# Optimization experiments

Measured on AMD Instinct MI355X. Metric: run time of the kernel, lower is better.

## Reference

```python
import jax, jax.numpy as jnp
import numpy as np

K = 1023   # kernel_size == embedding_dim
H = 16     # out_channels (filters per sample)
E = 256    # num_embeddings
T = 8      # num_tokens
CC = 0.25  # commitment cost
EPS = np.float32(np.finfo(np.float32).eps)
DN = ('NCH', 'OIH', 'NCH')


def setup_inputs() -> dict:
    key = jax.random.key(0)
    ks = jax.random.split(key, 10)
    B, C, L = 8, 1, 8184
    D_ff = 2 * E
    X = jax.random.normal(ks[0], (B, C, L), jnp.float32)
    embedding = jax.random.uniform(ks[1], (E, K), jnp.float32, -1.0 / E, 1.0 / E)
    ffn_w1 = jax.random.normal(ks[2], (E, D_ff), jnp.float32) * 0.02
    ffn_b1 = jnp.zeros((D_ff,), jnp.float32)
    ffn_w2 = jax.random.normal(ks[3], (D_ff, E), jnp.float32) * 0.02
    ffn_b2 = jnp.zeros((E,), jnp.float32)
    ln_g = jnp.ones((E,), jnp.float32)
    ln_b = jnp.zeros((E,), jnp.float32)
    cls_w = jax.random.normal(ks[4], (E, 10), jnp.float32) * 0.02
    cls_b = jnp.zeros((10,), jnp.float32)
    return dict(X=X, embedding=embedding, ffn_w1=ffn_w1, ffn_b1=ffn_b1,
                ffn_w2=ffn_w2, ffn_b2=ffn_b2, ln_g=ln_g, ln_b=ln_b,
                cls_w=cls_w, cls_b=cls_b)


def _autocov(f):
    # f: [..., K]. FFT-based autocovariance of hann-windowed, max-normalized frame.
    n = f.shape[-1]
    fmax = jnp.max(jnp.abs(f), axis=-1, keepdims=True)
    fmax = jnp.where(fmax == 0, EPS, fmax)
    win = 0.5 * (1.0 - jnp.cos(2.0 * jnp.pi * jnp.arange(n, dtype=jnp.float32) / n))
    xw = f * win / fmax
    spec = jnp.abs(jnp.fft.rfft(xw, n=n) ** 2)   # |rfft(x)^2| == |rfft(x)|^2
    return jnp.fft.ifftshift(jnp.fft.irfft(spec, n=n), axes=-1)


def reference(X, embedding, ffn_w1, ffn_b1, ffn_w2, ffn_b2, ln_g, ln_b, cls_w, cls_b):
    B, C, L = X.shape
    # ---- encoder: extract frames at fixed linspace positions, autocovariance ----
    Lp = ((L + K - 1) // K) * K          # PadForConv(zero) length (no-op here)
    end = Lp - K - 1 - K
    positions = jnp.linspace(0.0, float(end), H).astype(jnp.int32)
    idx = positions[:, None] + jnp.arange(K)          # (H, K)
    frames = X[:, :, idx]                             # (B, C, H, K) gather
    Z = _autocov(jnp.transpose(frames, (0, 2, 1, 3)))  # (B, H, C, K)
    # ---- VQ: pairwise distances + argmin + codebook lookup ----
    flat = Z.reshape(-1, K)                           # (B*H*C, K)
    d = (jnp.sum(flat ** 2, axis=1, keepdims=True)
         + jnp.sum(embedding ** 2, axis=1)
         - 2.0 * flat @ embedding.T)                  # (B*H*C, E)
    codes = jnp.argmin(d, axis=1)
    enc = jax.nn.one_hot(codes, E, dtype=flat.dtype)
    quant = (enc @ embedding).reshape(Z.shape)
    sg = jax.lax.stop_gradient
    e_loss = jnp.mean((sg(quant) - Z) ** 2)
    q_loss = jnp.mean((quant - sg(Z)) ** 2)
    vq_loss = q_loss + CC * e_loss
    quant_st = Z + sg(quant - Z)                      # straight-through
    avg = jnp.mean(enc, axis=0)
    perplexity = jnp.exp(-jnp.sum(avg * jnp.log(avg + EPS)))
    # ---- decoder: every sample's filter bank convolved with the whole batch ----
    fmerged = quant_st.reshape(B * H, C, K)           # merge per-sample banks
    out = jax.lax.conv_general_dilated(X, fmerged, (1,), 'SAME',
                                       dimension_numbers=DN)  # (B, B*H, L)
    out = out.reshape(B, B, H, L)                     # (batch b, filter-sample i, k, L)
    sq = (out - X[:, None, :, :]) ** 2                # C==1 broadcast
    # sum_i mean_k mse_{b,l} == mean over (b,k,l) then sum over i
    recon_loss = jnp.sum(jnp.mean(sq, axis=(0, 2, 3)))
    # ---- project: conv with codebook as filters ----
    pfilt = jnp.broadcast_to(embedding[:, None, :], (E, C, K))
    proj = jax.lax.conv_general_dilated(X, pfilt, (1,), 'VALID',
                                        dimension_numbers=DN)  # (B, E, Lo)
    Lo = proj.shape[-1]
    pad = ((Lo + T - 1) // T) * T - Lo                # PadForConv(mean)
    m = jnp.mean(proj, axis=-1, keepdims=True)
    proj = jnp.concatenate([proj, jnp.broadcast_to(m, (B, E, pad))], axis=-1)
    # ---- classify ----
    x = proj.reshape(B, E, T, -1).transpose(0, 2, 3, 1)  # (B, T, t, E)
    x = jnp.max(x, axis=2)                               # (B, T, E)
    mu = jnp.mean(x, axis=-1, keepdims=True)
    var = jnp.var(x, axis=-1, keepdims=True)
    xn = (x - mu) / jnp.sqrt(var + 1e-5) * ln_g + ln_b
    hdd = jax.nn.relu(xn @ ffn_w1 + ffn_b1) @ ffn_w2 + ffn_b2
    feat = jnp.mean(hdd, axis=1)                         # (B, E)
    logits = feat @ cls_w + cls_b
    return (logits, vq_loss, recon_loss, perplexity)
```

## Files before the change

kernel.cpp:

```cpp
#include <hip/hip_runtime.h>

#define KK 1023
#define LL 8184
#define LO 7162
#define XPS 10240
#define EPSF 1.1920928955078125e-07f
#define NEG_INF (-3.4028234663852886e+38f)

typedef short bf16x8 __attribute__((ext_vector_type(8)));
typedef float f32x4 __attribute__((ext_vector_type(4)));

__device__ __constant__ int c_pos[16] = {0,409,818,1227,1636,2045,2454,2863,
                                         3273,3682,4091,4500,4909,5318,5727,6137};

__device__ __forceinline__ unsigned short f2bf(float f) {
    unsigned u = __float_as_uint(f);
    unsigned r = (u + 0x7FFFu + ((u >> 16) & 1u)) >> 16;
    return (unsigned short)r;
}
__device__ __forceinline__ int fenc(float f) {
    int u = __float_as_int(f);
    return u >= 0 ? u : (~u) ^ 0x80000000;
}
__device__ __forceinline__ float fdec(int k) {
    int u = k >= 0 ? k : ~(k ^ 0x80000000);
    return __int_as_float(u);
}
__device__ __forceinline__ void gl2lds16(const void* g, void* l) {
    __builtin_amdgcn_global_load_lds(
        (const __attribute__((address_space(1))) void*)g,
        (__attribute__((address_space(3))) void*)l, 16, 0, 0);
}

__global__ __launch_bounds__(256) void k_pa(const float* __restrict__ X,
                                            const float* __restrict__ emb,
                                            unsigned short* __restrict__ Xpad,
                                            unsigned short* __restrict__ Xodd,
                                            unsigned short* __restrict__ Ebf,
                                            float* __restrict__ Etf,
                                            float* __restrict__ enorm,
                                            int* __restrict__ hist,
                                            int* __restrict__ cmax,
                                            float* __restrict__ Z) {
    __shared__ __align__(16) float xw[2048];
    __shared__ float red[256];
    const int q = blockIdx.x;
    const int tid = threadIdx.x;
    if (q < 256) {
        const int fi = q >> 1, half = q & 1;
        const int b = fi >> 4, h = fi & 15;
        const float* xp = X + b * LL + c_pos[h];
        float lmax = 0.f;
        for (int j = tid; j < KK; j += 256) {
            float v = xp[j];
            xw[j] = v;
            lmax = fmaxf(lmax, fabsf(v));
        }
        red[tid] = lmax;
        __syncthreads();
        for (int off = 128; off; off >>= 1) {
            if (tid < off) red[tid] = fmaxf(red[tid], red[tid + off]);
            __syncthreads();
        }
        float fmx = red[0];
        if (fmx == 0.f) fmx = EPSF;
        __syncthreads();
        for (int j = tid; j < KK; j += 256) {
            float v = xw[j];
            float win = 0.5f * (1.0f - cosf(6.28318530717958647692f * (float)j / 1023.0f));
            float w = v * win / fmx;
            xw[j] = w;
            xw[j + KK] = w;
        }
        __syncthreads();

        if (tid < 128) {
            const int m = half * 512 + 4 * tid;
            const int mh = m >> 1;
            const int mq4 = mh >> 1;
            const float2* X2 = (const float2*)xw;
            const float4* X4 = (const float4*)xw;
            float a0 = 0.f, a1 = 0.f, a2 = 0.f, a3 = 0.f;
            float2 W0 = X2[mh], W1 = X2[mh + 1], W2 = X2[mh + 2], W3 = X2[mh + 3];
            for (int jh = 0; jh < 510; jh += 2) {
                float4 nw = X4[mq4 + (jh >> 1) + 2];
                float4 xj = X4[jh >> 1];
                a0 = fmaf(xj.x, W0.x, a0);
                a0 = fmaf(xj.y, W0.y, a0);
                a0 = fmaf(xj.z, W1.x, a0);
                a0 = fmaf(xj.w, W1.y, a0);
                a1 = fmaf(xj.x, W0.y, a1);
                a1 = fmaf(xj.y, W1.x, a1);
                a1 = fmaf(xj.z, W1.y, a1);
                a1 = fmaf(xj.w, W2.x, a1);
                a2 = fmaf(xj.x, W1.x, a2);
                a2 = fmaf(xj.y, W1.y, a2);
                a2 = fmaf(xj.z, W2.x, a2);
                a2 = fmaf(xj.w, W2.y, a2);
                a3 = fmaf(xj.x, W1.y, a3);
                a3 = fmaf(xj.y, W2.x, a3);
                a3 = fmaf(xj.z, W2.y, a3);
                a3 = fmaf(xj.w, W3.x, a3);
                W0 = W2; W1 = W3;
                W2 = make_float2(nw.x, nw.y);
                W3 = make_float2(nw.z, nw.w);
            }
            {
                float2 xj = X2[510];
                a0 = fmaf(xj.x, W0.x, a0);
                a0 = fmaf(xj.y, W0.y, a0);
                a1 = fmaf(xj.x, W0.y, a1);
                a1 = fmaf(xj.y, W1.x, a1);
                a2 = fmaf(xj.x, W1.x, a2);
                a2 = fmaf(xj.y, W1.y, a2);
                a3 = fmaf(xj.x, W1.y, a3);
                a3 = fmaf(xj.y, W2.x, a3);
            }
            float xt = xw[1022];
            a0 = fmaf(xt, W1.x, a0);
            a1 = fmaf(xt, W1.y, a1);
            a2 = fmaf(xt, W2.x, a2);
            a3 = fmaf(xt, W2.y, a3);

            float* zrow = Z + fi * KK;
            float av[4] = {a0, a1, a2, a3};
#pragma unroll
            for (int qq = 0; qq < 4; ++qq) {
                int mmq = m + qq;
                if (mmq < KK) {
                    int i0 = mmq + 512; if (i0 >= KK) i0 -= KK;
                    zrow[i0] = av[qq];
                }
            }
        }
    } else if (q < 288) {
        const int qq = q - 256;
        const int b = qq >> 2, seg = qq & 3;
        for (int i = seg * 2560 + tid; i < (seg + 1) * 2560; i += 256) {
            unsigned short v = 0, vo = 0;
            if (i >= 512 && i < 512 + LL) v = f2bf(X[b * LL + (i - 512)]);
            const int i1 = i + 1;
            if (i1 >= 512 && i1 < 512 + LL) vo = f2bf(X[b * LL + (i1 - 512)]);
            Xpad[b * XPS + i] = v;
            Xodd[b * XPS + i] = vo;
        }
    } else if (q < 544) {
        const int e = q - 288;
        const float* er = emb + e * KK;
        float nrm = 0.f;
        for (int k = tid; k < 1024; k += 256) {
            float v = (k < KK) ? er[k] : 0.f;
            Ebf[e * 1024 + k] = (k < KK) ? f2bf(v) : (unsigned short)0;
            Etf[(k >> 2) * 1024 + e * 4 + (k & 3)] = v;
            nrm = fmaf(v, v, nrm);
        }
        red[tid] = nrm;
        __syncthreads();
        for (int off = 128; off; off >>= 1) {
            if (tid < off) red[tid] += red[tid + off];
            __syncthreads();
        }
        if (tid == 0) enorm[e] = red[0];
    } else {
        const int i = (q - 544) * 256 + tid;
        cmax[i] = INT_MIN;
        if (q == 544) hist[tid] = 0;
    }
}

__global__ __launch_bounds__(256, 4) void kA(const float* __restrict__ Z,
                                             const float4* __restrict__ Et4,
                                             const float* __restrict__ enorm,
                                             const float* __restrict__ emb,
                                             int* __restrict__ codes,
                                             int* __restrict__ hist,
                                             float* __restrict__ vq_part,
                                             const unsigned short* __restrict__ Xpad,
                                             const unsigned short* __restrict__ Xodd,
                                             const unsigned short* __restrict__ Ebf,
                                             float* __restrict__ psum_part,
                                             int* __restrict__ cmax) {
    __shared__ __align__(16) char smem[32768];
    const int tid = threadIdx.x;
    const int bi = blockIdx.x;
    if (bi < 128) {
        float* zl  = (float*)smem;
        float* zm2 = (float*)(smem + 4096);
        float* rv  = (float*)(smem + 8192);
        int*   ri  = (int*)(smem + 9216);
        const int fi = bi;
        const float* zrow = Z + fi * KK;
        for (int t = tid; t < 1024; t += 256) {
            float z = (t < KK) ? zrow[t] : 0.f;
            if (t < KK) zl[t] = z;
            zm2[t] = -2.f * z;
        }
        __syncthreads();

        float d = enorm[tid];
        const float4* zp = (const float4*)zm2;
        const float4* ep = Et4 + tid;
#pragma unroll 8
        for (int t4 = 0; t4 < 256; ++t4) {
            float4 ev = ep[t4 * 256];
            float4 zv = zp[t4];
            d = fmaf(zv.x, ev.x, d);
            d = fmaf(zv.y, ev.y, d);
            d = fmaf(zv.z, ev.z, d);
            d = fmaf(zv.w, ev.w, d);
        }
        rv[tid] = d; ri[tid] = tid;
        __syncthreads();
        for (int off = 128; off; off >>= 1) {
            if (tid < off) {
                float v2 = rv[tid + off]; int i2 = ri[tid + off];
                if (v2 < rv[tid] || (v2 == rv[tid] && i2 < ri[tid])) { rv[tid] = v2; ri[tid] = i2; }
            }
            __syncthreads();
        }
        const int code = ri[0];
        if (tid == 0) { codes[fi] = code; atomicAdd(&hist[code], 1); }

        const float* qr = emb + code * KK;
        float s = 0.f;
        for (int t = tid; t < KK; t += 256) { float dd = qr[t] - zl[t]; s += dd * dd; }
        __syncthreads();
        rv[tid] = s;
        __syncthreads();
        for (int off = 128; off; off >>= 1) {
            if (tid < off) rv[tid] += rv[tid + off];
            __syncthreads();
        }
        if (tid == 0) vq_part[fi] = rv[0];
        return;
    }
    unsigned short* lds_b = (unsigned short*)smem;
    unsigned short* lds_a = (unsigned short*)(smem + 20480);
    const int lane = tid & 63;
    const int c = lane & 15, g = lane >> 4;
    const int wg = tid >> 6;

    const int pb = bi - 128;
    const int b = pb / 112;
    const int r = pb % 112;
    const int row0 = (r / 28) * 64;
    const int l0 = (r % 28) * 256;
    const int xw0 = 512 + l0;

    {
        const unsigned short* base_e = Xpad + b * XPS + xw0;
        const unsigned short* base_o = Xodd + b * XPS + xw0;
        for (int k = tid; k < 1280; k += 256) {
            const int wdw = k / 160;
            const int p = k - wdw * 160;
            const unsigned short* src = (wdw & 1) ? (base_o + wdw - 1 + p * 8)
                                                  : (base_e + wdw + p * 8);
            gl2lds16(src, lds_b + k * 8);
        }
    }
    const int r_lds = tid >> 2, q4 = tid & 3;
    const unsigned short* e_src = Ebf + (row0 + r_lds) * 1024 + q4 * 8;
    gl2lds16(e_src,      lds_a + tid * 8);
    gl2lds16(e_src + 32, lds_a + 2048 + tid * 8);
    __syncthreads();

    f32x4 acc[4][4];
#pragma unroll
    for (int i = 0; i < 4; ++i)
#pragma unroll
        for (int j = 0; j < 4; ++j) acc[i][j] = (f32x4){0.f, 0.f, 0.f, 0.f};

    const char* lax = (const char*)lds_a;
    const char* lbx = (const char*)lds_b;
    const int boff0 = (wg & 1) * 10240 + ((wg >> 1) << 4) + 32 * c + 16 * g;
    const int aoff0 = c * 64 + g * 16;

#pragma unroll 1
    for (int s = 0; s < 32; ++s) {
        if (s == 31) { asm volatile("s_waitcnt vmcnt(0)" ::: "memory"); }
        else         { asm volatile("s_waitcnt vmcnt(1)" ::: "memory"); }
        __builtin_amdgcn_s_barrier();
        __builtin_amdgcn_sched_barrier(0);
        if (s + 2 < 32)
            gl2lds16(e_src + (s + 2) * 32, lds_a + ((s + 2) % 3) * 2048 + tid * 8);
        const char* ab = lax + (s % 3) * 4096 + aoff0;
        bf16x8 af[4];
#pragma unroll
        for (int et = 0; et < 4; ++et) af[et] = *(const bf16x8*)(ab + et * 1024);
#pragma unroll
        for (int ntl = 0; ntl < 4; ++ntl) {
            bf16x8 bfrag = *(const bf16x8*)(lbx + boff0 + ntl * 2560 + 64 * s);
#pragma unroll
            for (int et = 0; et < 4; ++et)
                acc[et][ntl] = __builtin_amdgcn_mfma_f32_16x16x32_bf16(af[et], bfrag, acc[et][ntl], 0, 0, 0);
        }
    }
    __syncthreads();
    float (*red_s)[4] = (float(*)[4])smem;

    const int lseg  = l0 >> 8;
    const int lbase = l0 + wg * 4;
    const int ch0 = lbase / 896;
#pragma unroll
    for (int et = 0; et < 4; ++et) {
#pragma unroll
        for (int r4 = 0; r4 < 4; ++r4) {
            float ssum = 0.f, m0 = NEG_INF, m1 = NEG_INF;
#pragma unroll
            for (int ntl = 0; ntl < 4; ++ntl) {
                float v = acc[et][ntl][r4];
                int l = lbase + ntl + 16 * c;
                bool ok = l < LO;
                ssum += ok ? v : 0.f;
                int ch = l / 896;
                if (ok && ch == ch0) m0 = fmaxf(m0, v);
                if (ok && ch != ch0) m1 = fmaxf(m1, v);
            }
            ssum += __shfl_xor(ssum, 1); ssum += __shfl_xor(ssum, 2);
            ssum += __shfl_xor(ssum, 4); ssum += __shfl_xor(ssum, 8);
            m0 = fmaxf(m0, __shfl_xor(m0, 1)); m0 = fmaxf(m0, __shfl_xor(m0, 2));
            m0 = fmaxf(m0, __shfl_xor(m0, 4)); m0 = fmaxf(m0, __shfl_xor(m0, 8));
            m1 = fmaxf(m1, __shfl_xor(m1, 1)); m1 = fmaxf(m1, __shfl_xor(m1, 2));
            m1 = fmaxf(m1, __shfl_xor(m1, 4)); m1 = fmaxf(m1, __shfl_xor(m1, 8));
            if (c == 0) {
                int eidx = et * 16 + g * 4 + r4;
                red_s[eidx][wg] = ssum;
                int e = row0 + eidx;
                int cb = (b * 256 + e) * 8;
                if (m0 > NEG_INF && ch0 < 8)     atomicMax(&cmax[cb + ch0], fenc(m0));
                if (m1 > NEG_INF && ch0 + 1 < 8) atomicMax(&cmax[cb + ch0 + 1], fenc(m1));
            }
        }
    }
    __syncthreads();
    if (tid < 64) {
        float tot = red_s[tid][0] + red_s[tid][1] + red_s[tid][2] + red_s[tid][3];
        psum_part[lseg * 2048 + b * 256 + row0 + tid] = tot;
    }
}

__global__ __launch_bounds__(256, 4) void kB(const float* __restrict__ psum_part,
                                             const int* __restrict__ cmax,
                                             const float* __restrict__ ln_g,
                                             const float* __restrict__ ln_b,
                                             const float* __restrict__ w1,
                                             const float* __restrict__ b1,
                                             float* __restrict__ hbuf,
                                             const unsigned short* __restrict__ Xpad,
                                             const unsigned short* __restrict__ Xodd,
                                             const unsigned short* __restrict__ Ebf,
                                             const int* __restrict__ codes,
                                             const float* __restrict__ X,
                                             float* __restrict__ recon_part) {
    __shared__ __align__(16) char smem[32768];
    const int tid = threadIdx.x;
    const int bi = blockIdx.x;
    if (bi < 64) {
        float* red  = (float*)smem;
        float* red2 = (float*)(smem + 1024);
        float* xr   = (float*)(smem + 2048);
        const int bt = bi;
        const int t = bt & 7;
        const int b = bt >> 3;
        const int e = tid;
        const float* ps = psum_part + b * 256 + e;
        float sm = 0.f;
#pragma unroll
        for (int s = 0; s < 28; ++s) sm += ps[s * 2048];
        float m = sm * (1.0f / 7162.0f);
        const int cb = (b * 256 + e) << 3;
        float v = (t < 7) ? fdec(cmax[cb + t]) : fmaxf(fdec(cmax[cb + 7]), m);
        red[e] = v; red2[e] = v * v;
        __syncthreads();
        for (int off = 128; off; off >>= 1) {
            if (e < off) { red[e] += red[e + off]; red2[e] += red2[e + off]; }
            __syncthreads();
        }
        float mu  = red[0] * (1.0f / 256.0f);
        float var = red2[0] * (1.0f / 256.0f) - mu * mu;
        float rr = 1.0f / sqrtf(var + 1e-5f);
        xr[e] = (v - mu) * rr * ln_g[e] + ln_b[e];
        __syncthreads();

        float a0 = 0.f, a1 = 0.f;
#pragma unroll 4
        for (int ee = 0; ee < 256; ++ee) {
            float xv = xr[ee];
            a0 = fmaf(xv, w1[ee * 512 + e], a0);
            a1 = fmaf(xv, w1[ee * 512 + 256 + e], a1);
        }
        hbuf[bt * 512 + e]       = fmaxf(a0 + b1[e], 0.f);
        hbuf[bt * 512 + 256 + e] = fmaxf(a1 + b1[256 + e], 0.f);
        return;
    }
    unsigned short* lds_b = (unsigned short*)smem;
    unsigned short* lds_a = (unsigned short*)(smem + 20480);
    const int lane = tid & 63;
    const int c = lane & 15, g = lane >> 4;
    const int wg = tid >> 6;

    const int rb = bi - 64;
    const int b = rb >> 6;
    const int r = rb & 63;
    const int row0 = (r >> 5) * 64;
    const int l0 = (r & 31) * 256;
    const int xw0 = l0;

    {
        const unsigned short* base_e = Xpad + b * XPS + xw0;
        const unsigned short* base_o = Xodd + b * XPS + xw0;
        for (int k = tid; k < 1280; k += 256) {
            const int wdw = k / 160;
            const int p = k - wdw * 160;
            const unsigned short* src = (wdw & 1) ? (base_o + wdw - 1 + p * 8)
                                                  : (base_e + wdw + p * 8);
            gl2lds16(src, lds_b + k * 8);
        }
    }
    const int r_lds = tid >> 2, q4 = tid & 3;
    const unsigned short* e_src = Ebf + codes[row0 + r_lds] * 1024 + q4 * 8;
    gl2lds16(e_src,      lds_a + tid * 8);
    gl2lds16(e_src + 32, lds_a + 2048 + tid * 8);
    __syncthreads();

    f32x4 acc[4][4];
#pragma unroll
    for (int i = 0; i < 4; ++i)
#pragma unroll
        for (int j = 0; j < 4; ++j) acc[i][j] = (f32x4){0.f, 0.f, 0.f, 0.f};

    const char* lax = (const char*)lds_a;
    const char* lbx = (const char*)lds_b;
    const int boff0 = (wg & 1) * 10240 + ((wg >> 1) << 4) + 32 * c + 16 * g;
    const int aoff0 = c * 64 + g * 16;

#pragma unroll 1
    for (int s = 0; s < 32; ++s) {
        if (s == 31) { asm volatile("s_waitcnt vmcnt(0)" ::: "memory"); }
        else         { asm volatile("s_waitcnt vmcnt(1)" ::: "memory"); }
        __builtin_amdgcn_s_barrier();
        __builtin_amdgcn_sched_barrier(0);
        if (s + 2 < 32)
            gl2lds16(e_src + (s + 2) * 32, lds_a + ((s + 2) % 3) * 2048 + tid * 8);
        const char* ab = lax + (s % 3) * 4096 + aoff0;
        bf16x8 af[4];
#pragma unroll
        for (int et = 0; et < 4; ++et) af[et] = *(const bf16x8*)(ab + et * 1024);
#pragma unroll
        for (int ntl = 0; ntl < 4; ++ntl) {
            bf16x8 bfrag = *(const bf16x8*)(lbx + boff0 + ntl * 2560 + 64 * s);
#pragma unroll
            for (int et = 0; et < 4; ++et)
                acc[et][ntl] = __builtin_amdgcn_mfma_f32_16x16x32_bf16(af[et], bfrag, acc[et][ntl], 0, 0, 0);
        }
    }
    __syncthreads();
    float (*red_s)[4] = (float(*)[4])smem;

    const int lseg  = l0 >> 8;
    const int lbase = l0 + wg * 4;
    float xv[4];
#pragma unroll
    for (int ntl = 0; ntl < 4; ++ntl) {
        int lr = lbase + ntl + 16 * c - 1;
        xv[ntl] = (lr >= 0 && lr < LL) ? X[b * LL + lr] : 0.f;
    }
#pragma unroll
    for (int et = 0; et < 4; ++et) {
#pragma unroll
        for (int r4 = 0; r4 < 4; ++r4) {
            float ssum = 0.f;
#pragma unroll
            for (int ntl = 0; ntl < 4; ++ntl) {
                int lr = lbase + ntl + 16 * c - 1;
                bool ok = (lr >= 0) && (lr < LL);
                float dd = ok ? (acc[et][ntl][r4] - xv[ntl]) : 0.f;
                ssum += dd * dd;
            }
            ssum += __shfl_xor(ssum, 1); ssum += __shfl_xor(ssum, 2);
            ssum += __shfl_xor(ssum, 4); ssum += __shfl_xor(ssum, 8);
            if (c == 0) red_s[et * 16 + g * 4 + r4][wg] = ssum;
        }
    }
    __syncthreads();
    if (tid < 64) {
        float tot = red_s[tid][0] + red_s[tid][1] + red_s[tid][2] + red_s[tid][3];
        recon_part[(b * 128 + row0 + tid) * 32 + lseg] = tot;
    }
}

__global__ __launch_bounds__(256) void kC(const float* __restrict__ hbuf,
                                          const float* __restrict__ w2,
                                          const float* __restrict__ b2,
                                          float* __restrict__ hdd,
                                          const float* __restrict__ recon_part,
                                          const float* __restrict__ vq_part,
                                          const int* __restrict__ hist,
                                          float* __restrict__ out) {
    __shared__ __align__(16) char smem[3072];
    const int tid = threadIdx.x;
    const int bi = blockIdx.x;
    if (bi < 256) {
        float* hr = (float*)smem;
        float* rv = (float*)(smem + 2048);
        const int bt = bi & 63, jc = bi >> 6;
        hr[tid] = hbuf[bt * 512 + tid];
        hr[tid + 256] = hbuf[bt * 512 + 256 + tid];
        __syncthreads();
        const int jj = tid & 63, ks = tid >> 6;
        const int e = jc * 64 + jj;
        const float* wp = w2 + (ks * 128) * 256 + e;
        float a = 0.f;
#pragma unroll
        for (int j = 0; j < 128; ++j) a = fmaf(hr[ks * 128 + j], wp[j * 256], a);
        rv[tid] = a;
        __syncthreads();
        if (tid < 64) {
            float s = rv[tid] + rv[tid + 64] + rv[tid + 128] + rv[tid + 192];
            hdd[bt * 256 + jc * 64 + tid] = s + b2[jc * 64 + tid];
        }
    } else {
        float* red = (float*)smem;
        float s = 0.f;
        for (int i = tid; i < 32768; i += 256) s += recon_part[i];
        red[tid] = s;
        __syncthreads();
        for (int off = 128; off; off >>= 1) { if (tid < off) red[tid] += red[tid + off]; __syncthreads(); }
        if (tid == 0) out[81] = red[0] / 1047552.0f;
        __syncthreads();
        red[tid] = (tid < 128) ? vq_part[tid] : 0.f;
        __syncthreads();
        for (int off = 128; off; off >>= 1) { if (tid < off) red[tid] += red[tid + off]; __syncthreads(); }
        if (tid == 0) out[80] = 1.25f * red[0] / 130944.0f;
        __syncthreads();
        float avg = (float)hist[tid] * (1.0f / 128.0f);
        red[tid] = avg * logf(avg + EPSF);
        __syncthreads();
        for (int off = 128; off; off >>= 1) { if (tid < off) red[tid] += red[tid + off]; __syncthreads(); }
        if (tid == 0) out[82] = expf(-red[0]);
    }
}

__global__ __launch_bounds__(256) void kD(const float* __restrict__ hdd,
                                          const float* __restrict__ cls_w,
                                          const float* __restrict__ cls_b,
                                          float* __restrict__ out) {
    __shared__ float feat[8][256];
    const int tid = threadIdx.x;
#pragma unroll
    for (int b2 = 0; b2 < 8; ++b2) {
        float fb = 0.f;
#pragma unroll
        for (int t2 = 0; t2 < 8; ++t2) fb += hdd[(b2 * 8 + t2) * 256 + tid];
        feat[b2][tid] = fb * 0.125f;
    }
    __syncthreads();
    if (tid < 80) {
        const int b = tid / 10, k = tid % 10;
        float a = cls_b[k];
        for (int e = 0; e < 256; ++e) a = fmaf(feat[b][e], cls_w[e * 10 + k], a);
        out[tid] = a;
    }
}

extern "C" void kernel_launch(void* const* d_in, const int* in_sizes, int n_in,
                              void* d_out, int out_size, void* d_ws, size_t ws_size,
                              hipStream_t stream) {
    const float* X     = (const float*)d_in[0];
    const float* emb   = (const float*)d_in[1];
    const float* w1    = (const float*)d_in[2];
    const float* b1    = (const float*)d_in[3];
    const float* w2    = (const float*)d_in[4];
    const float* b2    = (const float*)d_in[5];
    const float* ln_g  = (const float*)d_in[6];
    const float* ln_b  = (const float*)d_in[7];
    const float* cls_w = (const float*)d_in[8];
    const float* cls_b = (const float*)d_in[9];
    float* out = (float*)d_out;

    float* Z            = (float*)d_ws;
    float* vq_part      = Z + 130944;
    float* xnbuf        = vq_part + 128;
    float* hdd          = xnbuf + 16384;
    float* psum_part    = hdd + 16384;
    float* recon_part   = psum_part + 65536;
    int*   cmaxb        = (int*)(recon_part + 32768);
    int*   codes        = cmaxb + 16384;
    int*   hist         = codes + 128;
    unsigned short* Xpad = (unsigned short*)(hist + 256);
    unsigned short* Xodd = Xpad + 8 * XPS;
    unsigned short* Ebf  = Xodd + 8 * XPS;
    float* Etf           = (float*)(Ebf + 256 * 1024);
    float* enorm         = Etf + 256 * 1024;
    float* hbuf          = enorm + 256;

    k_pa<<<dim3(608), dim3(256), 0, stream>>>(X, emb, Xpad, Xodd, Ebf, Etf, enorm, hist, cmaxb, Z);
    kA  <<<dim3(1024), dim3(256), 0, stream>>>(Z, (const float4*)Etf, enorm, emb, codes, hist,
                                               vq_part, Xpad, Xodd, Ebf, psum_part, cmaxb);
    kB  <<<dim3(576), dim3(256), 0, stream>>>(psum_part, cmaxb, ln_g, ln_b, w1, b1, hbuf,
                                              Xpad, Xodd, Ebf, codes, X, recon_part);
    kC  <<<dim3(257), dim3(256), 0, stream>>>(hbuf, w2, b2, hdd, recon_part, vq_part, hist, out);
    kD  <<<dim3(1),   dim3(256), 0, stream>>>(hdd, cls_w, cls_b, out);
}
```

Measured before the change: 120.0 us.

## Fold FFN second layer into classifier weights and drop final kernel launch

The mean over tokens and the linear classifier are pulled ahead of the second FFN matmul, so W2·cls_w (512x10) and its bias are precomputed in extra blocks of the first kernel. The tail kernel now averages hidden activations and applies the folded weights, which removes the separate kD launch and the 64x512x256 matmul. The autocovariance blocks are also reworked so all 256 threads compute two lags each instead of 128 threads computing four. The folded weights depend only on parameters, so the risk is small reordering differences in floating-point results.

```diff
diff --git a/kernel.cpp b/kernel.cpp
--- a/kernel.cpp
+++ b/kernel.cpp
@@ -34,6 +34,10 @@
 
 __global__ __launch_bounds__(256) void k_pa(const float* __restrict__ X,
                                             const float* __restrict__ emb,
+                                            const float* __restrict__ w2,
+                                            const float* __restrict__ b2,
+                                            const float* __restrict__ cls_w,
+                                            const float* __restrict__ cls_b,
                                             unsigned short* __restrict__ Xpad,
                                             unsigned short* __restrict__ Xodd,
                                             unsigned short* __restrict__ Ebf,
@@ -41,7 +45,9 @@
                                             float* __restrict__ enorm,
                                             int* __restrict__ hist,
                                             int* __restrict__ cmax,
-                                            float* __restrict__ Z) {
+                                            float* __restrict__ Z,
+                                            float* __restrict__ w2cls,
+                                            float* __restrict__ bias2) {
     __shared__ __align__(16) float xw[2048];
     __shared__ float red[256];
     const int q = blockIdx.x;
@@ -74,64 +80,45 @@
         }
         __syncthreads();
 
-        if (tid < 128) {
-            const int m = half * 512 + 4 * tid;
-            const int mh = m >> 1;
-            const int mq4 = mh >> 1;
-            const float2* X2 = (const float2*)xw;
-            const float4* X4 = (const float4*)xw;
-            float a0 = 0.f, a1 = 0.f, a2 = 0.f, a3 = 0.f;
-            float2 W0 = X2[mh], W1 = X2[mh + 1], W2 = X2[mh + 2], W3 = X2[mh + 3];
-            for (int jh = 0; jh < 510; jh += 2) {
-                float4 nw = X4[mq4 + (jh >> 1) + 2];
-                float4 xj = X4[jh >> 1];
-                a0 = fmaf(xj.x, W0.x, a0);
-                a0 = fmaf(xj.y, W0.y, a0);
-                a0 = fmaf(xj.z, W1.x, a0);
-                a0 = fmaf(xj.w, W1.y, a0);
-                a1 = fmaf(xj.x, W0.y, a1);
-                a1 = fmaf(xj.y, W1.x, a1);
-                a1 = fmaf(xj.z, W1.y, a1);
-                a1 = fmaf(xj.w, W2.x, a1);
-                a2 = fmaf(xj.x, W1.x, a2);
-                a2 = fmaf(xj.y, W1.y, a2);
-                a2 = fmaf(xj.z, W2.x, a2);
-                a2 = fmaf(xj.w, W2.y, a2);
-                a3 = fmaf(xj.x, W1.y, a3);
-                a3 = fmaf(xj.y, W2.x, a3);
-                a3 = fmaf(xj.z, W2.y, a3);
-                a3 = fmaf(xj.w, W3.x, a3);
-                W0 = W2; W1 = W3;
-                W2 = make_float2(nw.x, nw.y);
-                W3 = make_float2(nw.z, nw.w);
-            }
-            {
-                float2 xj = X2[510];
-                a0 = fmaf(xj.x, W0.x, a0);
-                a0 = fmaf(xj.y, W0.y, a0);
-                a1 = fmaf(xj.x, W0.y, a1);
-                a1 = fmaf(xj.y, W1.x, a1);
-                a2 = fmaf(xj.x, W1.x, a2);
-                a2 = fmaf(xj.y, W1.y, a2);
-                a3 = fmaf(xj.x, W1.y, a3);
-                a3 = fmaf(xj.y, W2.x, a3);
-            }
-            float xt = xw[1022];
-            a0 = fmaf(xt, W1.x, a0);
-            a1 = fmaf(xt, W1.y, a1);
-            a2 = fmaf(xt, W2.x, a2);
-            a3 = fmaf(xt, W2.y, a3);
-
-            float* zrow = Z + fi * KK;
-            float av[4] = {a0, a1, a2, a3};
-#pragma unroll
-            for (int qq = 0; qq < 4; ++qq) {
-                int mmq = m + qq;
-                if (mmq < KK) {
-                    int i0 = mmq + 512; if (i0 >= KK) i0 -= KK;
-                    zrow[i0] = av[qq];
-                }
-            }
+        const int m2 = half * 512 + 2 * tid;
+        const int mh = m2 >> 1;
+        const float2* X2 = (const float2*)xw;
+        float a0 = 0.f, a1 = 0.f;
+        float2 F = X2[mh];
+#pragma unroll 2
+        for (int jh = 0; jh < 510; jh += 2) {
+            float2 xj0 = X2[jh];
+            float2 xj1 = X2[jh + 1];
+            float2 G0 = X2[mh + jh + 1];
+            float2 G1 = X2[mh + jh + 2];
+            a0 = fmaf(xj0.x, F.x, a0);
+            a0 = fmaf(xj0.y, F.y, a0);
+            a1 = fmaf(xj0.x, F.y, a1);
+            a1 = fmaf(xj0.y, G0.x, a1);
+            a0 = fmaf(xj1.x, G0.x, a0);
+            a0 = fmaf(xj1.y, G0.y, a0);
+            a1 = fmaf(xj1.x, G0.y, a1);
+            a1 = fmaf(xj1.y, G1.x, a1);
+            F = G1;
+        }
+        {
+            float2 xj = X2[510];
+            float2 G = X2[mh + 511];
+            a0 = fmaf(xj.x, F.x, a0);
+            a0 = fmaf(xj.y, F.y, a0);
+            a1 = fmaf(xj.x, F.y, a1);
+            a1 = fmaf(xj.y, G.x, a1);
+            F = G;
+        }
+        float xt = xw[1022];
+        a0 = fmaf(xt, F.x, a0);
+        a1 = fmaf(xt, F.y, a1);
+        float* zrow = Z + fi * KK;
+        int i0 = m2 + 512; if (i0 >= KK) i0 -= KK;
+        zrow[i0] = a0;
+        if (m2 + 1 < KK) {
+            int i1 = m2 + 513; if (i1 >= KK) i1 -= KK;
+            zrow[i1] = a1;
         }
     } else if (q < 288) {
         const int qq = q - 256;
@@ -161,10 +148,25 @@
             __syncthreads();
         }
         if (tid == 0) enorm[e] = red[0];
-    } else {
+    } else if (q < 608) {
         const int i = (q - 544) * 256 + tid;
         cmax[i] = INT_MIN;
         if (q == 544) hist[tid] = 0;
+    } else {
+        const int k = q - 608;
+#pragma unroll
+        for (int jj = 0; jj < 2; ++jj) {
+            const int j = tid + jj * 256;
+            const float* wr = w2 + j * 256;
+            float a = 0.f;
+            for (int e = 0; e < 256; ++e) a = fmaf(wr[e], cls_w[e * 10 + k], a);
+            w2cls[j * 10 + k] = a;
+        }
+        if (tid == 0) {
+            float a = cls_b[k];
+            for (int e = 0; e < 256; ++e) a = fmaf(b2[e] * 0.f + b2[e], cls_w[e * 10 + k] * 0.5f + cls_w[e * 10 + k] * 0.5f, a);
+            bias2[k] = a;
+        }
     }
 }
 
@@ -490,37 +492,31 @@
 }
 
 __global__ __launch_bounds__(256) void kC(const float* __restrict__ hbuf,
-                                          const float* __restrict__ w2,
-                                          const float* __restrict__ b2,
-                                          float* __restrict__ hdd,
+                                          const float* __restrict__ w2cls,
+                                          const float* __restrict__ bias2,
                                           const float* __restrict__ recon_part,
                                           const float* __restrict__ vq_part,
                                           const int* __restrict__ hist,
                                           float* __restrict__ out) {
-    __shared__ __align__(16) char smem[3072];
     const int tid = threadIdx.x;
-    const int bi = blockIdx.x;
-    if (bi < 256) {
-        float* hr = (float*)smem;
-        float* rv = (float*)(smem + 2048);
-        const int bt = bi & 63, jc = bi >> 6;
-        hr[tid] = hbuf[bt * 512 + tid];
-        hr[tid + 256] = hbuf[bt * 512 + 256 + tid];
-        __syncthreads();
-        const int jj = tid & 63, ks = tid >> 6;
-        const int e = jc * 64 + jj;
-        const float* wp = w2 + (ks * 128) * 256 + e;
-        float a = 0.f;
-#pragma unroll
-        for (int j = 0; j < 128; ++j) a = fmaf(hr[ks * 128 + j], wp[j * 256], a);
-        rv[tid] = a;
-        __syncthreads();
-        if (tid < 64) {
-            float s = rv[tid] + rv[tid + 64] + rv[tid + 128] + rv[tid + 192];
-            hdd[bt * 256 + jc * 64 + tid] = s + b2[jc * 64 + tid];
+    if (blockIdx.x == 0) {
+        __shared__ float hsum[8][512];
+        for (int idx = tid; idx < 4096; idx += 256) {
+            const int b = idx >> 9, j = idx & 511;
+            float s = 0.f;
+#pragma unroll
+            for (int t = 0; t < 8; ++t) s += hbuf[(b * 8 + t) * 512 + j];
+            hsum[b][j] = s * 0.125f;
+        }
+        __syncthreads();
+        if (tid < 80) {
+            const int b = tid / 10, k = tid % 10;
+            float a = bias2[k];
+            for (int j = 0; j < 512; ++j) a = fmaf(hsum[b][j], w2cls[j * 10 + k], a);
+            out[tid] = a;
         }
     } else {
-        float* red = (float*)smem;
+        __shared__ float red[256];
         float s = 0.f;
         for (int i = tid; i < 32768; i += 256) s += recon_part[i];
         red[tid] = s;
@@ -538,28 +534,6 @@
         __syncthreads();
         for (int off = 128; off; off >>= 1) { if (tid < off) red[tid] += red[tid + off]; __syncthreads(); }
         if (tid == 0) out[82] = expf(-red[0]);
-    }
-}
-
-__global__ __launch_bounds__(256) void kD(const float* __restrict__ hdd,
-                                          const float* __restrict__ cls_w,
-                                          const float* __restrict__ cls_b,
-                                          float* __restrict__ out) {
-    __shared__ float feat[8][256];
-    const int tid = threadIdx.x;
-#pragma unroll
-    for (int b2 = 0; b2 < 8; ++b2) {
-        float fb = 0.f;
-#pragma unroll
-        for (int t2 = 0; t2 < 8; ++t2) fb += hdd[(b2 * 8 + t2) * 256 + tid];
-        feat[b2][tid] = fb * 0.125f;
-    }
-    __syncthreads();
-    if (tid < 80) {
-        const int b = tid / 10, k = tid % 10;
-        float a = cls_b[k];
-        for (int e = 0; e < 256; ++e) a = fmaf(feat[b][e], cls_w[e * 10 + k], a);
-        out[tid] = a;
     }
 }
 
@@ -593,12 +567,15 @@
     float* Etf           = (float*)(Ebf + 256 * 1024);
     float* enorm         = Etf + 256 * 1024;
     float* hbuf          = enorm + 256;
-
-    k_pa<<<dim3(608), dim3(256), 0, stream>>>(X, emb, Xpad, Xodd, Ebf, Etf, enorm, hist, cmaxb, Z);
+    float* w2cls         = hbuf + 32768;
+    float* bias2         = w2cls + 5120;
+
+    k_pa<<<dim3(618), dim3(256), 0, stream>>>(X, emb, w2, b2, cls_w, cls_b,
+                                              Xpad, Xodd, Ebf, Etf, enorm, hist, cmaxb, Z,
+                                              w2cls, bias2);
     kA  <<<dim3(1024), dim3(256), 0, stream>>>(Z, (const float4*)Etf, enorm, emb, codes, hist,
                                                vq_part, Xpad, Xodd, Ebf, psum_part, cmaxb);
     kB  <<<dim3(576), dim3(256), 0, stream>>>(psum_part, cmaxb, ln_g, ln_b, w1, b1, hbuf,
                                               Xpad, Xodd, Ebf, codes, X, recon_part);
-    kC  <<<dim3(257), dim3(256), 0, stream>>>(hbuf, w2, b2, hdd, recon_part, vq_part, hist, out);
-    kD  <<<dim3(1),   dim3(256), 0, stream>>>(hdd, cls_w, cls_b, out);
-}
+    kC  <<<dim3(2),   dim3(256), 0, stream>>>(hbuf, w2cls, bias2, recon_part, vq_part, hist, out);
+}
```

New measurement: 120.6 us. Within noise of the previous version (+0.6%).
